# Kernel optimization log

Measured on AMD Instinct MI355X. Metric: run time of the kernel, lower is better.

## Reference

```python
import jax, jax.numpy as jnp
import numpy as np

MUL = 32          # multiplicity of 0e and 1o channels
NRAD = 8          # radial basis size
NPATH = 7         # TP instructions

# Orthonormal symmetric-traceless basis for the real l=2 irrep -> Cartesian map
_B = np.zeros((5, 3, 3))
_s2 = 1.0 / np.sqrt(2.0)
_B[0, 0, 1] = _B[0, 1, 0] = _s2                      # xy
_B[1, 1, 2] = _B[1, 2, 1] = _s2                      # yz
_B[2] = np.diag([-1.0, -1.0, 2.0]) / np.sqrt(6.0)    # 2z^2-x^2-y^2
_B[3, 0, 2] = _B[3, 2, 0] = _s2                      # xz
_B[4] = np.diag([1.0, -1.0, 0.0]) / np.sqrt(2.0)     # x^2-y^2
# w3j(1,2,1)[i,M,k], Frobenius-normalized to 1 (e3nn convention)
C121 = jnp.asarray(np.transpose(_B, (1, 0, 2)) / np.sqrt(5.0), jnp.float32)
INV_SQRT3 = float(1.0 / np.sqrt(3.0))   # w3j(1,1,0) / w3j(0,1,1) / w3j(1,0,1)
A0 = float(1.0 / np.sqrt(64.0))         # path weight, l=0 outs: sqrt(1/fan_in), fan_in=2*32
A1 = float(np.sqrt(3.0 / 96.0))         # path weight, l=1 out: sqrt((2l+1)/fan_in), fan_in=3*32


def setup_inputs() -> dict:
    key = jax.random.key(0)
    ks = jax.random.split(key, 9)
    N, E = 4096, 32768
    x = jax.random.normal(ks[0], (N, 4 * MUL), jnp.float32)
    edge_attr = jax.random.normal(ks[1], (E, 9), jnp.float32)
    edge_length = jax.random.uniform(ks[2], (E,), jnp.float32) * 5.0
    edge_src = jax.random.randint(ks[3], (E,), 0, N)
    edge_dst = jax.random.randint(ks[4], (E,), 0, N)
    W_fc1 = jax.random.normal(ks[5], (NRAD, 64), jnp.float32)
    W_fc2 = jax.random.normal(ks[6], (64, NPATH * MUL * MUL), jnp.float32)
    W_sc_s = jax.random.normal(ks[7], (MUL, MUL), jnp.float32)
    W_sc_v = jax.random.normal(ks[8], (MUL, MUL), jnp.float32)
    return dict(x=x, edge_attr=edge_attr, edge_length=edge_length,
                edge_src=edge_src, edge_dst=edge_dst,
                W_fc1=W_fc1, W_fc2=W_fc2, W_sc_s=W_sc_s, W_sc_v=W_sc_v)


def reference(x, edge_attr, edge_length, edge_src, edge_dst, W_fc1, W_fc2, W_sc_s, W_sc_v):
    N = x.shape[0]
    # radial Gaussian basis: centers linspace(0,5,8), sigma = spacing
    centers = jnp.linspace(0.0, 5.0, NRAD)
    sigma = 5.0 / (NRAD - 1)
    d = edge_length[:, None] - centers[None, :]
    radial = jnp.exp(-d * d / (2.0 * sigma * sigma))
    # radial MLP -> per-edge TP weights (e3nn FullyConnectedNet: W/sqrt(fan_in), silu)
    h = jax.nn.silu(radial @ (W_fc1 / jnp.sqrt(jnp.float32(NRAD))))
    w = h @ (W_fc2 / jnp.sqrt(jnp.float32(64)))          # [E, 7168]
    W = w.reshape(-1, NPATH, MUL, MUL)                    # [E,7,u,w]
    # split node features: 32x0e scalars + 32x1o vectors
    s = x[:, :MUL]
    v = x[:, MUL:].reshape(N, MUL, 3)
    sj = s[edge_src]                                      # [E,u]
    vj = v[edge_src]                                      # [E,u,3]
    y0 = edge_attr[:, 0]
    y1 = edge_attr[:, 1:4]
    y2 = edge_attr[:, 4:9]
    # tensor-product paths
    t00 = sj * y0[:, None]                                            # 0e x 0e
    t11 = jnp.einsum('eui,ei->eu', vj, y1) * INV_SQRT3                # 1o x 1o -> 0e
    out_s = (jnp.einsum('eu,euw->ew', t00, W[:, 0]) +
             jnp.einsum('eu,euw->ew', t11, W[:, 1])) * A0             # scalars
    out_g = (jnp.einsum('eu,euw->ew', t00, W[:, 2]) +
             jnp.einsum('eu,euw->ew', t11, W[:, 3])) * A0             # gates
    t01 = sj[:, :, None] * y1[:, None, :] * INV_SQRT3                 # 0e x 1o -> 1o
    t10 = vj * (y0[:, None, None] * INV_SQRT3)                        # 1o x 0e -> 1o
    t12 = jnp.einsum('eui,imk,em->euk', vj, C121, y2)                 # 1o x 2e -> 1o
    out_v = (jnp.einsum('euk,euw->ewk', t01, W[:, 4]) +
             jnp.einsum('euk,euw->ewk', t10, W[:, 5]) +
             jnp.einsum('euk,euw->ewk', t12, W[:, 6])) * A1           # [E,w,3]
    m_ij = jnp.concatenate([out_s, out_g, out_v.reshape(-1, 3 * MUL)], axis=1)  # [E,160]
    # scatter-mean over destination nodes
    sums = jax.ops.segment_sum(m_ij, edge_dst, num_segments=N)
    cnt = jax.ops.segment_sum(jnp.ones((m_ij.shape[0],), m_ij.dtype), edge_dst, num_segments=N)
    m_i = sums / jnp.clip(cnt, 1.0)[:, None]
    # gate: silu on scalars, sigmoid gates multiply the 1o block per-channel
    gs = jax.nn.silu(m_i[:, :MUL])
    gate = jax.nn.sigmoid(m_i[:, MUL:2 * MUL])
    gv = m_i[:, 2 * MUL:].reshape(N, MUL, 3) * gate[:, :, None]
    # residual self-connection (e3nn o3.Linear: per-irrep, / sqrt(mul_in))
    inv_sqrt_mul = 1.0 / jnp.sqrt(jnp.float32(MUL))
    h_s = gs + (s @ W_sc_s) * inv_sqrt_mul
    h_v = gv + jnp.einsum('nui,uw->nwi', v, W_sc_v) * inv_sqrt_mul
    # o3.Norm: per-irrep L2 norm over the (2l+1) components
    norm_s = jnp.sqrt(h_s * h_s + 1e-12)
    norm_v = jnp.sqrt(jnp.sum(h_v * h_v, axis=-1) + 1e-12)
    return jnp.concatenate([norm_s, norm_v], axis=1)       # [N, 64]
```

## Files before the change

### kernel.cpp

```cpp
#include <hip/hip_runtime.h>

#define NIVL  256
#define KINV  51.2f
#define KSTEP 0.01953125f
#define TPW   7168
#define BCAP  256
#define DCAP  64
#define NROW  11
#define TSTR  40
#define PREPT 455

typedef __attribute__((ext_vector_type(8))) __bf16 bf16x8;
typedef __attribute__((ext_vector_type(4))) float f32x4;
union FragU { uint4 u; bf16x8 v; };

__device__ __forceinline__ float sigmoidf_(float v) { return 1.f / (1.f + expf(-v)); }
__device__ __forceinline__ unsigned bf16r_(float x) { return (__float_as_uint(x) + 0x8000u) >> 16; }
__device__ __forceinline__ unsigned pk_(float lo, float hi) { return (bf16r_(hi) << 16) | bf16r_(lo); }

__device__ __forceinline__ f32x4 mfma_(bf16x8 a, bf16x8 b, f32x4 c) {
    return __builtin_amdgcn_mfma_f32_16x16x32_bf16(a, b, c, 0, 0, 0);
}

__global__ __launch_bounds__(256)
void prep_kernel(const float* __restrict__ W1, const float* __restrict__ W2,
                 const float* __restrict__ elen, const int* __restrict__ esrc,
                 const int* __restrict__ edst, const float* __restrict__ ea,
                 float* __restrict__ T, int* __restrict__ cntL, int* __restrict__ cntD,
                 float* __restrict__ erec, int* __restrict__ sortedD, int E)
{
    const int tid = threadIdx.x;
    if (blockIdx.x < PREPT) {
        __shared__ float hk_s[4][64];
        const int bx = blockIdx.x % 7;
        const int k0 = (blockIdx.x / 7) * 4;
        const int pw = bx * 1024 + tid * 4;
        {
            int kk = tid >> 6, c = tid & 63;
            float L = (float)(k0 + kk) * KSTEP;
            float d = 0.f;
#pragma unroll
            for (int r = 0; r < 8; ++r) {
                float dd = L - (float)r * (5.f / 7.f);
                d += expf(-dd * dd * 0.98f) * W1[r * 64 + c];
            }
            d *= 0.3535533906f;
            hk_s[kk][c] = d * sigmoidf_(d) * 0.125f;
        }
        __syncthreads();
        float4 acc[4];
#pragma unroll
        for (int q = 0; q < 4; ++q) acc[q] = make_float4(0.f, 0.f, 0.f, 0.f);
#pragma unroll 4
        for (int c = 0; c < 64; ++c) {
            float4 w4 = *(const float4*)(W2 + (size_t)c * TPW + pw);
#pragma unroll
            for (int q = 0; q < 4; ++q) {
                float hv = hk_s[q][c];
                acc[q].x = fmaf(hv, w4.x, acc[q].x);
                acc[q].y = fmaf(hv, w4.y, acc[q].y);
                acc[q].z = fmaf(hv, w4.z, acc[q].z);
                acc[q].w = fmaf(hv, w4.w, acc[q].w);
            }
        }
#pragma unroll
        for (int q = 0; q < 4; ++q) {
            int k = k0 + q;
            if (k < 257)
                *(float4*)(T + (size_t)k * TPW + pw) = acc[q];
        }
    } else {
        const float I3 = 0.5773502692f, I5 = 0.4472135955f, S2 = 0.7071067812f;
        const float I6 = 0.4082482905f, T6 = 0.8164965809f;
        int e = (blockIdx.x - PREPT) * 256 + tid;
        if (e < E) {
            float t = elen[e] * KINV;
            int j = (int)t; j = j > 255 ? 255 : j;
            int pos = atomicAdd(&cntL[j], 1);
            if (pos < BCAP) {
                const float* y = ea + (size_t)e * 9;
                float y0 = y[0];
                float a = y[4], b = y[5], c = y[6], d2 = y[7], ee = y[8];
                float4 r0, r1, r2, r3;
                r0.x = t - (float)j;
                r0.y = __int_as_float(esrc[e]);
                r0.z = __int_as_float(e);
                r0.w = y0;
                r1.x = y0 * I3;
                r1.y = y[1] * I3; r1.z = y[2] * I3; r1.w = y[3] * I3;
                r2.x = (-c * I6 + ee * S2) * I5;
                r2.y = a * S2 * I5;
                r2.z = d2 * S2 * I5;
                r2.w = (-c * I6 - ee * S2) * I5;
                r3.x = b * S2 * I5;
                r3.y = c * T6 * I5;
                r3.z = 0.f; r3.w = 0.f;
                float4* dst = (float4*)(erec + ((size_t)j * BCAP + pos) * 16);
                dst[0] = r0; dst[1] = r1; dst[2] = r2; dst[3] = r3;
            }
            int d = edst[e];
            int pd = atomicAdd(&cntD[d], 1);
            if (pd < DCAP) sortedD[d * DCAP + pd] = e;
        }
    }
}

__global__ __launch_bounds__(256)
void pack_kernel(const float* __restrict__ T, uint4* __restrict__ Bpk)
{
    const int j = blockIdx.x;
    const int tid = threadIdx.x;
    const float* Trow  = T + (size_t)j * TPW;
    const float* Trow2 = Trow + TPW;
    uint4* bp = Bpk + (size_t)j * 28 * 64;
    for (int i = tid; i < 896; i += 256) {
        int pl = i >> 7, rem = i & 127;
        int whs = rem >> 6, lane_s = rem & 63;
        int u0 = (lane_s >> 4) * 8, w = whs * 16 + (lane_s & 15);
        int basei = pl * 1024 + w;
        unsigned ta[4], dd[4];
#pragma unroll
        for (int q = 0; q < 4; ++q) {
            float a0 = Trow[basei + (u0 + 2 * q) * 32];
            float a1 = Trow[basei + (u0 + 2 * q + 1) * 32];
            float b0 = Trow2[basei + (u0 + 2 * q) * 32];
            float b1 = Trow2[basei + (u0 + 2 * q + 1) * 32];
            ta[q] = pk_(a0, a1);
            dd[q] = pk_(b0 - a0, b1 - a1);
        }
        bp[(pl * 4 + whs) * 64 + lane_s]     = make_uint4(ta[0], ta[1], ta[2], ta[3]);
        bp[(pl * 4 + 2 + whs) * 64 + lane_s] = make_uint4(dd[0], dd[1], dd[2], dd[3]);
    }
}

__global__ __launch_bounds__(256, 2)
void fold_kernel(const float* __restrict__ x, const int* __restrict__ cntL,
                 const float* __restrict__ erec, const uint4* __restrict__ Bpk,
                 float* __restrict__ msg)
{
    const int j = blockIdx.x >> 1, half = blockIdx.x & 1;
    __shared__ __align__(16) unsigned short TB[2 * NROW * 16 * TSTR];
    __shared__ float ECF[32];
    __shared__ int   ECE[32];
    const int tid = threadIdx.x;

    const int cnt = min(cntL[j], BCAP);
    const int nchunk = (cnt + 31) >> 5;
    const int te = tid & 31, sub = tid >> 5;
    const int wv = tid >> 6, lane = tid & 63;
    const int sg = wv >> 1, wh = wv & 1;
    const int col = lane & 15, quad = lane >> 4;

    float4 er0 = {0,0,0,0}, er1 = {0,0,0,0}, er2 = {0,0,0,0}, er3 = {0,0,0,0};
    if (half < nchunk) {
        int ce = min(32, cnt - (half << 5));
        if (te < ce) {
            const float4* rp = (const float4*)(erec + ((size_t)j * BCAP + (half << 5) + te) * 16);
            er0 = rp[0]; er1 = rp[1]; er2 = rp[2]; er3 = rp[3];
        }
    }

    bf16x8 Bt[7][2];
    {
        const uint4* bp = Bpk + (size_t)j * 28 * 64 + lane;
#pragma unroll
        for (int pl = 0; pl < 7; ++pl) {
            FragU fa; fa.u = bp[(pl * 4 + wh) * 64];     Bt[pl][0] = fa.v;
            FragU fd; fd.u = bp[(pl * 4 + 2 + wh) * 64]; Bt[pl][1] = fd.v;
        }
    }

    const float A0 = 0.125f, A1 = 0.1767766953f;

    for (int ci = half; ci < nchunk; ci += 2) {
        const int base = ci << 5;
        const int cntE = min(32, cnt - base);

        const int u0 = sub * 4;
        float s4[4], vv[12];
        if (te < cntE) {
            int src = __float_as_int(er0.y);
            const float* xp = x + (size_t)src * 128;
            *(float4*)s4 = *(const float4*)(xp + u0);
            *(float4*)(vv)     = *(const float4*)(xp + 32 + 3 * u0);
            *(float4*)(vv + 4) = *(const float4*)(xp + 32 + 3 * u0 + 4);
            *(float4*)(vv + 8) = *(const float4*)(xp + 32 + 3 * u0 + 8);
        }
        float4 nr0 = {0,0,0,0}, nr1 = {0,0,0,0}, nr2 = {0,0,0,0}, nr3 = {0,0,0,0};
        const int cin = ci + 2;
        if (cin < nchunk) {
            int ce2 = min(32, cnt - (cin << 5));
            if (te < ce2) {
                const float4* rp = (const float4*)(erec + ((size_t)j * BCAP + (cin << 5) + te) * 16);
                nr0 = rp[0]; nr1 = rp[1]; nr2 = rp[2]; nr3 = rp[3];
            }
        }

        __syncthreads();

        {
            const int esg = te >> 4, e16 = te & 15;
            float rv[NROW][4];
            if (te < cntE) {
                float y0 = er0.w;
                float y0i = er1.x, y1i0 = er1.y, y1i1 = er1.z, y1i2 = er1.w;
                float M0 = er2.x, M1 = er2.y, M2 = er2.z, M4 = er2.w;
                float M5 = er3.x, M8 = er3.y;
                if (sub == 0) {
                    ECF[te] = er0.x;
                    ECE[te] = __float_as_int(er0.z);
                }
#pragma unroll
                for (int up = 0; up < 4; ++up) {
                    float s = s4[up];
                    float v0 = vv[3 * up], v1 = vv[3 * up + 1], v2 = vv[3 * up + 2];
                    rv[0][up] = s * y0;
                    rv[1][up] = v0 * y1i0 + v1 * y1i1 + v2 * y1i2;
                    rv[2][up] = s * y1i0;
                    rv[3][up] = s * y1i1;
                    rv[4][up] = s * y1i2;
                    rv[5][up] = v0 * y0i;
                    rv[6][up] = v1 * y0i;
                    rv[7][up] = v2 * y0i;
                    rv[8][up]  = v0 * M0 + v1 * M1 + v2 * M2;
                    rv[9][up]  = v0 * M1 + v1 * M4 + v2 * M5;
                    rv[10][up] = v0 * M2 + v1 * M5 + v2 * M8;
                }
            } else {
#pragma unroll
                for (int r = 0; r < NROW; ++r)
#pragma unroll
                    for (int up = 0; up < 4; ++up) rv[r][up] = 0.f;
            }
#pragma unroll
            for (int r = 0; r < NROW; ++r) {
                unsigned lo = pk_(rv[r][0], rv[r][1]);
                unsigned hi = pk_(rv[r][2], rv[r][3]);
                *(uint2*)&TB[((esg * NROW + r) * 16 + e16) * TSTR + u0] = make_uint2(lo, hi);
            }
        }
        __syncthreads();

        f32x4 cS0 = {0,0,0,0}, cS1 = {0,0,0,0}, cG0 = {0,0,0,0}, cG1 = {0,0,0,0};
        f32x4 cV[3][2];
#pragma unroll
        for (int k = 0; k < 3; ++k) { cV[k][0] = (f32x4){0,0,0,0}; cV[k][1] = (f32x4){0,0,0,0}; }

        #define LOADA(r) ({ FragU fa_; fa_.u = *(const uint4*)&TB[((sg * NROW + (r)) * 16 + col) * TSTR + quad * 8]; fa_.v; })

        bf16x8 a0 = LOADA(0), a1 = LOADA(1);
        cS0 = mfma_(a0, Bt[0][0], cS0); cS0 = mfma_(a1, Bt[1][0], cS0);
        cS1 = mfma_(a0, Bt[0][1], cS1); cS1 = mfma_(a1, Bt[1][1], cS1);
        cG0 = mfma_(a0, Bt[2][0], cG0); cG0 = mfma_(a1, Bt[3][0], cG0);
        cG1 = mfma_(a0, Bt[2][1], cG1); cG1 = mfma_(a1, Bt[3][1], cG1);
#pragma unroll
        for (int k = 0; k < 3; ++k) {
            bf16x8 ak;
            ak = LOADA(2 + k);
            cV[k][0] = mfma_(ak, Bt[4][0], cV[k][0]);
            cV[k][1] = mfma_(ak, Bt[4][1], cV[k][1]);
            ak = LOADA(5 + k);
            cV[k][0] = mfma_(ak, Bt[5][0], cV[k][0]);
            cV[k][1] = mfma_(ak, Bt[5][1], cV[k][1]);
            ak = LOADA(8 + k);
            cV[k][0] = mfma_(ak, Bt[6][0], cV[k][0]);
            cV[k][1] = mfma_(ak, Bt[6][1], cV[k][1]);
        }

        const int w = wh * 16 + col;
#pragma unroll
        for (int reg = 0; reg < 4; ++reg) {
            int e = sg * 16 + quad * 4 + reg;
            if (e < cntE) {
                float f = ECF[e];
                int eid = ECE[e];
                float* mp = msg + (size_t)eid * 160;
                mp[w]            = (cS0[reg] + f * cS1[reg]) * A0;
                mp[32 + w]       = (cG0[reg] + f * cG1[reg]) * A0;
                mp[64 + 3 * w]     = (cV[0][0][reg] + f * cV[0][1][reg]) * A1;
                mp[64 + 3 * w + 1] = (cV[1][0][reg] + f * cV[1][1][reg]) * A1;
                mp[64 + 3 * w + 2] = (cV[2][0][reg] + f * cV[2][1][reg]) * A1;
            }
        }
        #undef LOADA
        er0 = nr0; er1 = nr1; er2 = nr2; er3 = nr3;
    }
}

__global__ __launch_bounds__(256)
void node_kernel(const float* __restrict__ x, const float* __restrict__ Wss,
                 const float* __restrict__ Wsv, const float* __restrict__ msg,
                 const int* __restrict__ sortedD, const int* __restrict__ cntD,
                 float* __restrict__ out, int N)
{
    __shared__ float ms[8][160];
    const int tid = threadIdx.x;
    const int n0 = blockIdx.x * 8;
    const float IM = 0.1767766953f;

#pragma unroll
    for (int it = 0; it < 5; ++it) {
        int task = tid + it * 256;
        int nl = task / 160;
        int c = task - nl * 160;
        int n = n0 + nl;
        if (n < N) {
            int cd = cntD[n];
            int cc = cd < DCAP ? cd : DCAP;
            const int* sp = sortedD + n * DCAP;
            float s = 0.f;
            for (int i0 = 0; i0 < cc; i0 += 8) {
                int4 ia = *(const int4*)(sp + i0);
                int4 ib = *(const int4*)(sp + i0 + 4);
                int id[8] = { ia.x, ia.y, ia.z, ia.w, ib.x, ib.y, ib.z, ib.w };
                float p[8];
#pragma unroll
                for (int k = 0; k < 8; ++k)
                    p[k] = (i0 + k < cc) ? msg[(size_t)id[k] * 160 + c] : 0.f;
#pragma unroll
                for (int k = 0; k < 8; ++k) s += p[k];
            }
            ms[nl][c] = s / fmaxf((float)cd, 1.f);
        }
    }
    __syncthreads();

#pragma unroll
    for (int it = 0; it < 2; ++it) {
        int task = tid + it * 256;
        int nl = task >> 6, col = task & 63;
        int n = n0 + nl;
        if (n >= N) continue;
        const float* m  = ms[nl];
        const float* xp = x + (size_t)n * 128;
        if (col < 32) {
            int w = col;
            float mval = m[w];
            float gs = mval * sigmoidf_(mval);
            float dot = 0.f;
#pragma unroll 4
            for (int u = 0; u < 32; ++u) dot += xp[u] * Wss[u * 32 + w];
            float hs = gs + dot * IM;
            out[(size_t)n * 64 + w] = sqrtf(hs * hs + 1e-12f);
        } else {
            int w = col - 32;
            float gate = sigmoidf_(m[32 + w]);
            float g0 = m[64 + 3 * w + 0] * gate;
            float g1 = m[64 + 3 * w + 1] * gate;
            float g2 = m[64 + 3 * w + 2] * gate;
            float d0 = 0.f, d1 = 0.f, d2 = 0.f;
#pragma unroll 4
            for (int u = 0; u < 32; ++u) {
                float wv = Wsv[u * 32 + w];
                d0 += xp[32 + 3 * u + 0] * wv;
                d1 += xp[32 + 3 * u + 1] * wv;
                d2 += xp[32 + 3 * u + 2] * wv;
            }
            float h0 = g0 + d0 * IM, h1 = g1 + d1 * IM, h2 = g2 + d2 * IM;
            out[(size_t)n * 64 + 32 + w] = sqrtf(h0 * h0 + h1 * h1 + h2 * h2 + 1e-12f);
        }
    }
}

extern "C" void kernel_launch(void* const* d_in, const int* in_sizes, int n_in,
                              void* d_out, int out_size, void* d_ws, size_t ws_size,
                              hipStream_t stream)
{
    const float* x    = (const float*)d_in[0];
    const float* ea   = (const float*)d_in[1];
    const float* elen = (const float*)d_in[2];
    const int*   esrc = (const int*)d_in[3];
    const int*   edst = (const int*)d_in[4];
    const float* W1   = (const float*)d_in[5];
    const float* W2   = (const float*)d_in[6];
    const float* Wss  = (const float*)d_in[7];
    const float* Wsv  = (const float*)d_in[8];
    float* out = (float*)d_out;

    const int N = in_sizes[0] / 128;
    const int E = in_sizes[2];

    float* T      = (float*)d_ws;
    float* Bpkf   = T + (size_t)257 * TPW;
    float* msg    = Bpkf + (size_t)256 * 28 * 64 * 4;
    float* erec   = msg + (size_t)E * 160;
    int*   cntL   = (int*)(erec + (size_t)256 * BCAP * 16);
    int*   cntD   = cntL + 256;
    int*   sortedD= cntD + N;
    uint4* Bpk    = (uint4*)Bpkf;

    hipMemsetAsync(cntL, 0, (size_t)(256 + N) * sizeof(int), stream);

    prep_kernel<<<PREPT + (E + 255) / 256, 256, 0, stream>>>(W1, W2, elen, esrc, edst, ea, T, cntL, cntD, erec, sortedD, E);
    pack_kernel<<<NIVL, 256, 0, stream>>>(T, Bpk);
    fold_kernel<<<NIVL * 2, 256, 0, stream>>>(x, cntL, erec, Bpk, msg);
    node_kernel<<<(N + 7) / 8, 256, 0, stream>>>(x, Wss, Wsv, msg, sortedD, cntD, out, N);
}
```

Measured before the change: 139.9 us.

## Fuse bf16 packing into prep kernel and index messages by bucket slot

The separate pack kernel and the fp32 T table in global memory are removed. Each prep block now computes 5 consecutive radial rows (one overlap row) into shared memory and packs the bf16 base and delta fragments straight into Bpk. Messages are also stored by bucket slot instead of edge id, with sortedD recording slots, so fold no longer needs the ECE edge-id table and writes contiguously. This saves one launch and a global round trip of T, at the cost of about 25% redundant FMA work for the overlap row and more shared memory per block.

```diff
diff --git a/kernel.cpp b/kernel.cpp
--- a/kernel.cpp
+++ b/kernel.cpp
@@ -8,7 +8,7 @@
 #define DCAP  64
 #define NROW  11
 #define TSTR  40
-#define PREPT 455
+#define TPACK 448
 
 typedef __attribute__((ext_vector_type(8))) __bf16 bf16x8;
 typedef __attribute__((ext_vector_type(4))) float f32x4;
@@ -26,17 +26,18 @@
 void prep_kernel(const float* __restrict__ W1, const float* __restrict__ W2,
                  const float* __restrict__ elen, const int* __restrict__ esrc,
                  const int* __restrict__ edst, const float* __restrict__ ea,
-                 float* __restrict__ T, int* __restrict__ cntL, int* __restrict__ cntD,
+                 uint4* __restrict__ Bpk, int* __restrict__ cntL, int* __restrict__ cntD,
                  float* __restrict__ erec, int* __restrict__ sortedD, int E)
 {
+    __shared__ float hk_s[5][64];
+    __shared__ float Tsl[5][1024];
     const int tid = threadIdx.x;
-    if (blockIdx.x < PREPT) {
-        __shared__ float hk_s[4][64];
-        const int bx = blockIdx.x % 7;
-        const int k0 = (blockIdx.x / 7) * 4;
-        const int pw = bx * 1024 + tid * 4;
-        {
-            int kk = tid >> 6, c = tid & 63;
+    const int vb = blockIdx.x;
+    if (vb < TPACK) {
+        const int bx = vb % 7;
+        const int k0 = (vb / 7) * 4;
+        for (int idx = tid; idx < 320; idx += 256) {
+            int kk = idx >> 6, c = idx & 63;
             float L = (float)(k0 + kk) * KSTEP;
             float d = 0.f;
 #pragma unroll
@@ -48,14 +49,15 @@
             hk_s[kk][c] = d * sigmoidf_(d) * 0.125f;
         }
         __syncthreads();
-        float4 acc[4];
-#pragma unroll
-        for (int q = 0; q < 4; ++q) acc[q] = make_float4(0.f, 0.f, 0.f, 0.f);
+        float4 acc[5];
+#pragma unroll
+        for (int q = 0; q < 5; ++q) acc[q] = make_float4(0.f, 0.f, 0.f, 0.f);
+        const int pw = bx * 1024 + tid * 4;
 #pragma unroll 4
         for (int c = 0; c < 64; ++c) {
             float4 w4 = *(const float4*)(W2 + (size_t)c * TPW + pw);
 #pragma unroll
-            for (int q = 0; q < 4; ++q) {
+            for (int q = 0; q < 5; ++q) {
                 float hv = hk_s[q][c];
                 acc[q].x = fmaf(hv, w4.x, acc[q].x);
                 acc[q].y = fmaf(hv, w4.y, acc[q].y);
@@ -63,16 +65,34 @@
                 acc[q].w = fmaf(hv, w4.w, acc[q].w);
             }
         }
-#pragma unroll
-        for (int q = 0; q < 4; ++q) {
-            int k = k0 + q;
-            if (k < 257)
-                *(float4*)(T + (size_t)k * TPW + pw) = acc[q];
+        __syncthreads();
+#pragma unroll
+        for (int q = 0; q < 5; ++q)
+            *(float4*)&Tsl[q][tid * 4] = acc[q];
+        __syncthreads();
+        const int lane_s = tid & 63, whs = (tid >> 6) & 1, ih = tid >> 7;
+        const int u0p = (lane_s >> 4) * 8, wp = whs * 16 + (lane_s & 15);
+#pragma unroll
+        for (int t2 = 0; t2 < 2; ++t2) {
+            const int jj = k0 + ih + t2 * 2;
+            const int kk = jj - k0;
+            unsigned ta[4], dd[4];
+#pragma unroll
+            for (int q = 0; q < 4; ++q) {
+                float a0 = Tsl[kk][(u0p + 2 * q) * 32 + wp];
+                float a1 = Tsl[kk][(u0p + 2 * q + 1) * 32 + wp];
+                float b0 = Tsl[kk + 1][(u0p + 2 * q) * 32 + wp];
+                float b1 = Tsl[kk + 1][(u0p + 2 * q + 1) * 32 + wp];
+                ta[q] = pk_(a0, a1);
+                dd[q] = pk_(b0 - a0, b1 - a1);
+            }
+            Bpk[((size_t)jj * 28 + bx * 4 + whs) * 64 + lane_s]     = make_uint4(ta[0], ta[1], ta[2], ta[3]);
+            Bpk[((size_t)jj * 28 + bx * 4 + 2 + whs) * 64 + lane_s] = make_uint4(dd[0], dd[1], dd[2], dd[3]);
         }
     } else {
         const float I3 = 0.5773502692f, I5 = 0.4472135955f, S2 = 0.7071067812f;
         const float I6 = 0.4082482905f, T6 = 0.8164965809f;
-        int e = (blockIdx.x - PREPT) * 256 + tid;
+        int e = (vb - TPACK) * 256 + tid;
         if (e < E) {
             float t = elen[e] * KINV;
             int j = (int)t; j = j > 255 ? 255 : j;
@@ -84,7 +104,7 @@
                 float4 r0, r1, r2, r3;
                 r0.x = t - (float)j;
                 r0.y = __int_as_float(esrc[e]);
-                r0.z = __int_as_float(e);
+                r0.z = 0.f;
                 r0.w = y0;
                 r1.x = y0 * I3;
                 r1.y = y[1] * I3; r1.z = y[2] * I3; r1.w = y[3] * I3;
@@ -98,38 +118,11 @@
                 float4* dst = (float4*)(erec + ((size_t)j * BCAP + pos) * 16);
                 dst[0] = r0; dst[1] = r1; dst[2] = r2; dst[3] = r3;
             }
+            int slot = j * BCAP + (pos < BCAP ? pos : BCAP - 1);
             int d = edst[e];
             int pd = atomicAdd(&cntD[d], 1);
-            if (pd < DCAP) sortedD[d * DCAP + pd] = e;
-        }
-    }
-}
-
-__global__ __launch_bounds__(256)
-void pack_kernel(const float* __restrict__ T, uint4* __restrict__ Bpk)
-{
-    const int j = blockIdx.x;
-    const int tid = threadIdx.x;
-    const float* Trow  = T + (size_t)j * TPW;
-    const float* Trow2 = Trow + TPW;
-    uint4* bp = Bpk + (size_t)j * 28 * 64;
-    for (int i = tid; i < 896; i += 256) {
-        int pl = i >> 7, rem = i & 127;
-        int whs = rem >> 6, lane_s = rem & 63;
-        int u0 = (lane_s >> 4) * 8, w = whs * 16 + (lane_s & 15);
-        int basei = pl * 1024 + w;
-        unsigned ta[4], dd[4];
-#pragma unroll
-        for (int q = 0; q < 4; ++q) {
-            float a0 = Trow[basei + (u0 + 2 * q) * 32];
-            float a1 = Trow[basei + (u0 + 2 * q + 1) * 32];
-            float b0 = Trow2[basei + (u0 + 2 * q) * 32];
-            float b1 = Trow2[basei + (u0 + 2 * q + 1) * 32];
-            ta[q] = pk_(a0, a1);
-            dd[q] = pk_(b0 - a0, b1 - a1);
-        }
-        bp[(pl * 4 + whs) * 64 + lane_s]     = make_uint4(ta[0], ta[1], ta[2], ta[3]);
-        bp[(pl * 4 + 2 + whs) * 64 + lane_s] = make_uint4(dd[0], dd[1], dd[2], dd[3]);
+            if (pd < DCAP) sortedD[d * DCAP + pd] = slot;
+        }
     }
 }
 
@@ -141,7 +134,6 @@
     const int j = blockIdx.x >> 1, half = blockIdx.x & 1;
     __shared__ __align__(16) unsigned short TB[2 * NROW * 16 * TSTR];
     __shared__ float ECF[32];
-    __shared__ int   ECE[32];
     const int tid = threadIdx.x;
 
     const int cnt = min(cntL[j], BCAP);
@@ -177,14 +169,14 @@
         const int cntE = min(32, cnt - base);
 
         const int u0 = sub * 4;
-        float s4[4], vv[12];
+        float s4[4], vvx[12];
         if (te < cntE) {
             int src = __float_as_int(er0.y);
             const float* xp = x + (size_t)src * 128;
             *(float4*)s4 = *(const float4*)(xp + u0);
-            *(float4*)(vv)     = *(const float4*)(xp + 32 + 3 * u0);
-            *(float4*)(vv + 4) = *(const float4*)(xp + 32 + 3 * u0 + 4);
-            *(float4*)(vv + 8) = *(const float4*)(xp + 32 + 3 * u0 + 8);
+            *(float4*)(vvx)     = *(const float4*)(xp + 32 + 3 * u0);
+            *(float4*)(vvx + 4) = *(const float4*)(xp + 32 + 3 * u0 + 4);
+            *(float4*)(vvx + 8) = *(const float4*)(xp + 32 + 3 * u0 + 8);
         }
         float4 nr0 = {0,0,0,0}, nr1 = {0,0,0,0}, nr2 = {0,0,0,0}, nr3 = {0,0,0,0};
         const int cin = ci + 2;
@@ -206,14 +198,11 @@
                 float y0i = er1.x, y1i0 = er1.y, y1i1 = er1.z, y1i2 = er1.w;
                 float M0 = er2.x, M1 = er2.y, M2 = er2.z, M4 = er2.w;
                 float M5 = er3.x, M8 = er3.y;
-                if (sub == 0) {
-                    ECF[te] = er0.x;
-                    ECE[te] = __float_as_int(er0.z);
-                }
+                if (sub == 0) ECF[te] = er0.x;
 #pragma unroll
                 for (int up = 0; up < 4; ++up) {
                     float s = s4[up];
-                    float v0 = vv[3 * up], v1 = vv[3 * up + 1], v2 = vv[3 * up + 2];
+                    float v0 = vvx[3 * up], v1 = vvx[3 * up + 1], v2 = vvx[3 * up + 2];
                     rv[0][up] = s * y0;
                     rv[1][up] = v0 * y1i0 + v1 * y1i1 + v2 * y1i2;
                     rv[2][up] = s * y1i0;
@@ -268,13 +257,13 @@
         }
 
         const int w = wh * 16 + col;
+        const int sbase = j * BCAP + base;
 #pragma unroll
         for (int reg = 0; reg < 4; ++reg) {
             int e = sg * 16 + quad * 4 + reg;
             if (e < cntE) {
                 float f = ECF[e];
-                int eid = ECE[e];
-                float* mp = msg + (size_t)eid * 160;
+                float* mp = msg + (size_t)(sbase + e) * 160;
                 mp[w]            = (cS0[reg] + f * cS1[reg]) * A0;
                 mp[32 + w]       = (cG0[reg] + f * cG1[reg]) * A0;
                 mp[64 + 3 * w]     = (cV[0][0][reg] + f * cV[0][1][reg]) * A1;
@@ -351,10 +340,10 @@
             float d0 = 0.f, d1 = 0.f, d2 = 0.f;
 #pragma unroll 4
             for (int u = 0; u < 32; ++u) {
-                float wv = Wsv[u * 32 + w];
-                d0 += xp[32 + 3 * u + 0] * wv;
-                d1 += xp[32 + 3 * u + 1] * wv;
-                d2 += xp[32 + 3 * u + 2] * wv;
+                float wvv = Wsv[u * 32 + w];
+                d0 += xp[32 + 3 * u + 0] * wvv;
+                d1 += xp[32 + 3 * u + 1] * wvv;
+                d2 += xp[32 + 3 * u + 2] * wvv;
             }
             float h0 = g0 + d0 * IM, h1 = g1 + d1 * IM, h2 = g2 + d2 * IM;
             out[(size_t)n * 64 + 32 + w] = sqrtf(h0 * h0 + h1 * h1 + h2 * h2 + 1e-12f);
@@ -380,10 +369,9 @@
     const int N = in_sizes[0] / 128;
     const int E = in_sizes[2];
 
-    float* T      = (float*)d_ws;
-    float* Bpkf   = T + (size_t)257 * TPW;
+    float* Bpkf   = (float*)d_ws;
     float* msg    = Bpkf + (size_t)256 * 28 * 64 * 4;
-    float* erec   = msg + (size_t)E * 160;
+    float* erec   = msg + (size_t)256 * BCAP * 160;
     int*   cntL   = (int*)(erec + (size_t)256 * BCAP * 16);
     int*   cntD   = cntL + 256;
     int*   sortedD= cntD + N;
@@ -391,8 +379,7 @@
 
     hipMemsetAsync(cntL, 0, (size_t)(256 + N) * sizeof(int), stream);
 
-    prep_kernel<<<PREPT + (E + 255) / 256, 256, 0, stream>>>(W1, W2, elen, esrc, edst, ea, T, cntL, cntD, erec, sortedD, E);
-    pack_kernel<<<NIVL, 256, 0, stream>>>(T, Bpk);
+    prep_kernel<<<TPACK + (E + 255) / 256, 256, 0, stream>>>(W1, W2, elen, esrc, edst, ea, Bpk, cntL, cntD, erec, sortedD, E);
     fold_kernel<<<NIVL * 2, 256, 0, stream>>>(x, cntL, erec, Bpk, msg);
     node_kernel<<<(N + 7) / 8, 256, 0, stream>>>(x, Wss, Wsv, msg, sortedD, cntD, out, N);
 }
```

After: 134.1 us (median of 2 runs). -4.1%, faster.
